# Kernel tuning notes

Hardware: AMD Instinct MI355X
Metric: run time of the kernel (lower is better)

## Reference

```python
import jax, jax.numpy as jnp
import numpy as np

DECAY = 0.99
EPSILON = 1e-05


def setup_inputs() -> dict:
    key = jax.random.key(0)
    k1, k2, k3, k4 = jax.random.split(key, 4)
    B, S, D, K = 16, 2048, 512, 2048
    x = jax.random.normal(k1, (B, S, D), dtype=jnp.float32)
    embed = jax.random.normal(k2, (K, D), dtype=jnp.float32)
    cluster_size = jax.random.uniform(k3, (K,), dtype=jnp.float32)
    embed_avg = jax.random.normal(k4, (K, D), dtype=jnp.float32)
    return {"x": x, "embed": embed, "cluster_size": cluster_size, "embed_avg": embed_avg}


def reference(x, embed, cluster_size, embed_avg):
    # x: [B,S,D]  embed: [K,D]  cluster_size: [K]  embed_avg: [K,D]
    B, S, D = x.shape
    K = embed.shape[0]
    xf = x.reshape(-1, D)  # [N,D], N=B*S

    # quantize(): negative squared euclidean distance, argmax over codebook
    x_sq = jnp.sum(xf * xf, axis=1, keepdims=True)            # [N,1]
    e_sq = jnp.sum(embed * embed, axis=1)[None, :]            # [1,K]
    dist = -(x_sq - 2.0 * (xf @ embed.T) + e_sq)              # [N,K]
    embed_ind = jnp.argmax(dist, axis=-1)                     # [N] int

    # dequantize
    quantize = embed[embed_ind].reshape(B, S, D)

    # training EMA updates (onehot.sum(0) and x^T @ onehot expressed as segment sums)
    ones = jnp.ones((xf.shape[0],), dtype=x.dtype)
    bins = jax.ops.segment_sum(ones, embed_ind, num_segments=K)        # [K] == onehot.sum(0)
    embed_sum_t = jax.ops.segment_sum(xf, embed_ind, num_segments=K)   # [K,D] == (x.T @ onehot).T

    new_cluster_size = cluster_size * DECAY + (1.0 - DECAY) * bins
    new_embed_avg = embed_avg * DECAY + (1.0 - DECAY) * embed_sum_t

    total = new_cluster_size.sum()
    smoothed = (new_cluster_size + EPSILON) / (total + K * EPSILON) * total  # laplace smoothing
    new_embed = new_embed_avg / smoothed[:, None]

    return (quantize,
            embed_ind.reshape(B, S),
            dist.reshape(B, S, K),
            new_cluster_size,
            new_embed_avg,
            new_embed)
```

## Files before the change

### kernel.cpp

```cpp
#include <hip/hip_runtime.h>

#define DECAY 0.99f
#define OMD   0.01f
#define EPS   1e-5f

constexpr int Bb = 16, Ss = 2048, Dd = 512, Kk = 2048;
constexpr int Nn = Bb * Ss;

typedef __attribute__((ext_vector_type(8))) short short8;
typedef __attribute__((ext_vector_type(4))) float f32x4;

__device__ __forceinline__ unsigned short f2bf(float x) {
    unsigned u = __float_as_uint(x);
    unsigned r = (u + 0x7FFFu + ((u >> 16) & 1u)) >> 16;
    return (unsigned short)r;
}
__device__ __forceinline__ float bf2f(unsigned short u) {
    return __uint_as_float((unsigned)u << 16);
}

__device__ __forceinline__ void gload_lds16(const void* g, void* l) {
    __builtin_amdgcn_global_load_lds(
        (const __attribute__((address_space(1))) void*)g,
        (__attribute__((address_space(3))) void*)l, 16, 0, 0);
}

#define BARRIER() do { asm volatile("" ::: "memory"); \
                       __builtin_amdgcn_s_barrier();  \
                       asm volatile("" ::: "memory"); } while (0)

__global__ void rows_sq(const float* __restrict__ in, float* __restrict__ out, int nrows) {
    int row  = blockIdx.x * 4 + (threadIdx.x >> 6);
    int lane = threadIdx.x & 63;
    if (row >= nrows) return;
    const float4* p = (const float4*)(in + (size_t)row * Dd);
    float s = 0.f;
    #pragma unroll
    for (int i = 0; i < 2; ++i) {
        float4 v = p[lane + 64 * i];
        s += v.x * v.x + v.y * v.y + v.z * v.z + v.w * v.w;
    }
    #pragma unroll
    for (int off = 32; off; off >>= 1) s += __shfl_down(s, off);
    if (lane == 0) out[row] = s;
}

__global__ void conv_split2(const float* __restrict__ in,
                            unsigned short* __restrict__ ph,
                            unsigned short* __restrict__ pm, int n4) {
    int i = blockIdx.x * 256 + threadIdx.x;
    if (i >= n4) return;
    float4 v = ((const float4*)in)[i];
    float f[4] = {v.x, v.y, v.z, v.w};
    ushort4 h, m;
    unsigned short hh[4], mm[4];
    #pragma unroll
    for (int j = 0; j < 4; ++j) {
        float x = f[j];
        unsigned short a = f2bf(x);  float ra = x - bf2f(a);
        unsigned short b = f2bf(ra);
        hh[j] = a; mm[j] = b;
    }
    h.x = hh[0]; h.y = hh[1]; h.z = hh[2]; h.w = hh[3];
    m.x = mm[0]; m.y = mm[1]; m.z = mm[2]; m.w = mm[3];
    ((ushort4*)ph)[i] = h;
    ((ushort4*)pm)[i] = m;
}

__global__ __launch_bounds__(512, 1) void gemm_split256(
    const unsigned short* __restrict__ xp,
    const unsigned short* __restrict__ ep,
    const float* __restrict__ xsq,
    const float* __restrict__ esq,
    float* __restrict__ dist,
    unsigned long long* __restrict__ packed)
{
    __shared__ unsigned short As[2][256][64];
    __shared__ unsigned short Bs[2][256][64];

    const int tid  = threadIdx.x;
    const int lane = tid & 63;
    const int wid  = tid >> 6;
    const int wr   = wid >> 2;
    const int wc   = wid & 3;

    int bid = blockIdx.x;
    int wg  = (bid & 7) * 128 + (bid >> 3);
    int mb  = wg >> 3, nb = wg & 7;
    const int row0 = mb * 256, col0 = nb * 256;

    f32x4 acc[8][4] = {};
    short8 af[4], afh[4], bl[2], blh[2], bh[2], bhh[2];

    const int l8   = lane >> 3;
    const int csrc = (lane & 7) ^ l8;

    auto stageAt = [&](const unsigned short* pl, int d, int tt) {
        int ko = (tt & 7) * 64;
        #pragma unroll
        for (int jj = 0; jj < 4; ++jj) {
            int rowbase = jj * 64 + wid * 8;
            const unsigned short* src =
                pl + (size_t)(row0 + rowbase + l8) * Dd + ko + csrc * 8;
            gload_lds16(src, &As[d][rowbase][0]);
        }
    };
    auto stageBt = [&](const unsigned short* pl, int d, int tt) {
        int ko = (tt & 7) * 64;
        #pragma unroll
        for (int jj = 0; jj < 4; ++jj) {
            int rowbase = jj * 64 + wid * 8;
            const unsigned short* src =
                pl + (size_t)(col0 + rowbase + l8) * Dd + ko + csrc * 8;
            gload_lds16(src, &Bs[d][rowbase][0]);
        }
    };

    auto readA4 = [&](int d, int msel) {
        #pragma unroll
        for (int m = 0; m < 4; ++m) {
            int r  = wr * 128 + (msel * 4 + m) * 16 + (lane & 15);
            int c  = ((lane >> 4))     ^ (r & 7);
            int c2 = ((lane >> 4) + 4) ^ (r & 7);
            af[m]  = *(const short8*)&As[d][r][c * 8];
            afh[m] = *(const short8*)&As[d][r][c2 * 8];
        }
    };
    auto readBlo = [&](int d) {
        #pragma unroll
        for (int n = 0; n < 2; ++n) {
            int r  = wc * 64 + n * 16 + (lane & 15);
            int c  = ((lane >> 4))     ^ (r & 7);
            int c2 = ((lane >> 4) + 4) ^ (r & 7);
            bl[n]  = *(const short8*)&Bs[d][r][c * 8];
            blh[n] = *(const short8*)&Bs[d][r][c2 * 8];
        }
    };
    auto readBhi = [&](int d) {
        #pragma unroll
        for (int n = 0; n < 2; ++n) {
            int r  = wc * 64 + (2 + n) * 16 + (lane & 15);
            int c  = ((lane >> 4))     ^ (r & 7);
            int c2 = ((lane >> 4) + 4) ^ (r & 7);
            bh[n]  = *(const short8*)&Bs[d][r][c * 8];
            bhh[n] = *(const short8*)&Bs[d][r][c2 * 8];
        }
    };

    auto mfmaQ = [&](int msel, int nsel, const short8* b0, const short8* b1) {
        #pragma unroll
        for (int m = 0; m < 4; ++m)
            #pragma unroll
            for (int n = 0; n < 2; ++n) {
                int am = msel * 4 + m, bn = nsel * 2 + n;
                acc[am][bn] = __builtin_amdgcn_mfma_f32_16x16x32_bf16(af[m], b0[n], acc[am][bn], 0, 0, 0);
            }
        #pragma unroll
        for (int m = 0; m < 4; ++m)
            #pragma unroll
            for (int n = 0; n < 2; ++n) {
                int am = msel * 4 + m, bn = nsel * 2 + n;
                acc[am][bn] = __builtin_amdgcn_mfma_f32_16x16x32_bf16(afh[m], b1[n], acc[am][bn], 0, 0, 0);
            }
    };

    stageAt(xp, 0, 0);
    stageBt(ep, 0, 0);
    asm volatile("s_waitcnt vmcnt(0)" ::: "memory");
    BARRIER();

    for (int t = 0; t < 32; ++t) {
        const int cur = t & 1, nxt = cur ^ 1;
        const bool st = (t < 31);
        int pn = (t + 1) >> 3;
        const unsigned short* Apn = xp + (size_t)((pn == 2 || pn == 3) ? 1 : 0) * ((size_t)Nn * Dd);
        const unsigned short* Bpn = ep + (size_t)((pn == 1 || pn == 3) ? 1 : 0) * ((size_t)Kk * Dd);

        readA4(cur, 0); readBlo(cur); readBhi(cur);
        if (st) { stageAt(Apn, nxt, t + 1); stageBt(Bpn, nxt, t + 1); }
        mfmaQ(0, 0, bl, blh);
        mfmaQ(0, 1, bh, bhh);
        readA4(cur, 1);
        mfmaQ(1, 1, bh, bhh);
        mfmaQ(1, 0, bl, blh);
        asm volatile("s_waitcnt vmcnt(0)" ::: "memory");
        BARRIER();
    }

    const int jrow = (lane >> 4) * 4;
    const int ncol = lane & 15;
    #pragma unroll
    for (int m = 0; m < 8; ++m) {
        int rbase = row0 + wr * 128 + m * 16 + jrow;
        #pragma unroll
        for (int j = 0; j < 4; ++j) {
            int row = rbase + j;
            float xs = xsq[row];
            float best = -3.4e38f; int bi = 0;
            #pragma unroll
            for (int n = 0; n < 4; ++n) {
                int col = col0 + wc * 64 + n * 16 + ncol;
                float v = 2.f * acc[m][n][j] - xs - esq[col];
                dist[(size_t)row * Kk + col] = v;
                if (v > best) { best = v; bi = col; }
            }
            unsigned u = __float_as_uint(best);
            u = (u & 0x80000000u) ? ~u : (u | 0x80000000u);
            unsigned long long pk = ((unsigned long long)u << 32) | (unsigned)(~bi);
            #pragma unroll
            for (int off = 1; off < 16; off <<= 1) {
                unsigned long long o = __shfl_xor(pk, off);
                if (o > pk) pk = o;
            }
            if (ncol == 0) atomicMax(&packed[row], pk);
        }
    }
}

__global__ void unpack_argmax(const unsigned long long* __restrict__ packed,
                              float* __restrict__ ind_f, int* __restrict__ ind_i) {
    int i = blockIdx.x * 256 + threadIdx.x;
    unsigned long long p = packed[i];
    int k = (int)(~(unsigned)(p & 0xFFFFFFFFull));
    ind_f[i] = (float)k;
    ind_i[i] = k;
}

#define BM 64
#define BN 64
#define BK 32
__global__ __launch_bounds__(256) void gemm_dist(
    const float* __restrict__ A, const float* __restrict__ Bm,
    const float* __restrict__ xsq, const float* __restrict__ esq,
    float* __restrict__ dist)
{
    __shared__ float Asl[BK][BM + 4];
    __shared__ float Bsl[BK][BN + 4];
    int tid = threadIdx.x;
    int row0 = blockIdx.x * BM, col0 = blockIdx.y * BN;
    int tx = tid & 15, ty = tid >> 4;
    float acc[4][4] = {};
    int lr = tid >> 3, lc = (tid & 7) * 4;
    for (int d0 = 0; d0 < Dd; d0 += BK) {
        float4 a0 = *(const float4*)(A  + (size_t)(row0 + lr)      * Dd + d0 + lc);
        float4 a1 = *(const float4*)(A  + (size_t)(row0 + lr + 32) * Dd + d0 + lc);
        float4 b0 = *(const float4*)(Bm + (size_t)(col0 + lr)      * Dd + d0 + lc);
        float4 b1 = *(const float4*)(Bm + (size_t)(col0 + lr + 32) * Dd + d0 + lc);
        __syncthreads();
        Asl[lc + 0][lr] = a0.x; Asl[lc + 1][lr] = a0.y; Asl[lc + 2][lr] = a0.z; Asl[lc + 3][lr] = a0.w;
        Asl[lc + 0][lr + 32] = a1.x; Asl[lc + 1][lr + 32] = a1.y; Asl[lc + 2][lr + 32] = a1.z; Asl[lc + 3][lr + 32] = a1.w;
        Bsl[lc + 0][lr] = b0.x; Bsl[lc + 1][lr] = b0.y; Bsl[lc + 2][lr] = b0.z; Bsl[lc + 3][lr] = b0.w;
        Bsl[lc + 0][lr + 32] = b1.x; Bsl[lc + 1][lr + 32] = b1.y; Bsl[lc + 2][lr + 32] = b1.z; Bsl[lc + 3][lr + 32] = b1.w;
        __syncthreads();
        #pragma unroll
        for (int kd = 0; kd < BK; ++kd) {
            float4 av = *(const float4*)&Asl[kd][ty * 4];
            float4 bv = *(const float4*)&Bsl[kd][tx * 4];
            float a[4] = {av.x, av.y, av.z, av.w};
            float b[4] = {bv.x, bv.y, bv.z, bv.w};
            #pragma unroll
            for (int i = 0; i < 4; ++i)
                #pragma unroll
                for (int j = 0; j < 4; ++j)
                    acc[i][j] = fmaf(a[i], b[j], acc[i][j]);
        }
    }
    #pragma unroll
    for (int i = 0; i < 4; ++i) {
        int row = row0 + ty * 4 + i;
        float xs = xsq[row];
        float4 o;
        int col = col0 + tx * 4;
        o.x = 2.f * acc[i][0] - xs - esq[col + 0];
        o.y = 2.f * acc[i][1] - xs - esq[col + 1];
        o.z = 2.f * acc[i][2] - xs - esq[col + 2];
        o.w = 2.f * acc[i][3] - xs - esq[col + 3];
        *(float4*)(dist + (size_t)row * Kk + col) = o;
    }
}

__global__ void argmax_k(const float* __restrict__ dist,
                         float* __restrict__ ind_f, int* __restrict__ ind_i) {
    int row  = blockIdx.x * 4 + (threadIdx.x >> 6);
    int lane = threadIdx.x & 63;
    const float4* p = (const float4*)(dist + (size_t)row * Kk);
    float best = -3.4e38f;
    int bidx = 0;
    #pragma unroll
    for (int it = 0; it < Kk / 4 / 64; ++it) {
        int i = lane + it * 64;
        float4 v = p[i];
        int base = i * 4;
        if (v.x > best) { best = v.x; bidx = base + 0; }
        if (v.y > best) { best = v.y; bidx = base + 1; }
        if (v.z > best) { best = v.z; bidx = base + 2; }
        if (v.w > best) { best = v.w; bidx = base + 3; }
    }
    #pragma unroll
    for (int off = 32; off; off >>= 1) {
        float ov = __shfl_down(best, off);
        int   oi = __shfl_down(bidx, off);
        if (ov > best || (ov == best && oi < bidx)) { best = ov; bidx = oi; }
    }
    if (lane == 0) { ind_f[row] = (float)bidx; ind_i[row] = bidx; }
}

__global__ void gather_scatter(const float* __restrict__ x,
                               const float* __restrict__ embed,
                               const int* __restrict__ ind,
                               float* __restrict__ quant,
                               float* __restrict__ esum,
                               int* __restrict__ bins) {
    int n = blockIdx.x;
    int k = ind[n];
    int t = threadIdx.x;
    size_t xb = (size_t)n * Dd;
    size_t eb = (size_t)k * Dd;
    float v0 = x[xb + t];
    float v1 = x[xb + t + 256];
    quant[xb + t]       = embed[eb + t];
    quant[xb + t + 256] = embed[eb + t + 256];
    atomicAdd(&esum[eb + t],       v0);
    atomicAdd(&esum[eb + t + 256], v1);
    if (t == 0) atomicAdd(&bins[k], 1);
}

__global__ void finalize1(const float* __restrict__ cs, const int* __restrict__ bins,
                          float* __restrict__ ncs, float* __restrict__ total_ws) {
    __shared__ float red[16];
    int t = threadIdx.x;
    float s = 0.f;
    for (int k = t; k < Kk; k += 1024) {
        float v = cs[k] * DECAY + OMD * (float)bins[k];
        ncs[k] = v;
        s += v;
    }
    #pragma unroll
    for (int off = 32; off; off >>= 1) s += __shfl_down(s, off);
    if ((t & 63) == 0) red[t >> 6] = s;
    __syncthreads();
    if (t == 0) {
        float tot = 0.f;
        #pragma unroll
        for (int i = 0; i < 16; ++i) tot += red[i];
        total_ws[0] = tot;
    }
}

__global__ void finalize2(const float* __restrict__ ea, const float* __restrict__ esum,
                          const float* __restrict__ ncs, const float* __restrict__ total_ws,
                          float* __restrict__ nea, float* __restrict__ ne) {
    int idx = blockIdx.x * 256 + threadIdx.x;
    float total = total_ws[0];
    int k = idx >> 7;
    float sm = (ncs[k] + EPS) / (total + Kk * EPS) * total;
    float inv = 1.f / sm;
    float4 a = ((const float4*)ea)[idx];
    float4 s = ((const float4*)esum)[idx];
    float4 r;
    r.x = a.x * DECAY + OMD * s.x;
    r.y = a.y * DECAY + OMD * s.y;
    r.z = a.z * DECAY + OMD * s.z;
    r.w = a.w * DECAY + OMD * s.w;
    ((float4*)nea)[idx] = r;
    float4 e;
    e.x = r.x * inv; e.y = r.y * inv; e.z = r.z * inv; e.w = r.w * inv;
    ((float4*)ne)[idx] = e;
}

extern "C" void kernel_launch(void* const* d_in, const int* in_sizes, int n_in,
                              void* d_out, int out_size, void* d_ws, size_t ws_size,
                              hipStream_t stream) {
    const float* x     = (const float*)d_in[0];
    const float* embed = (const float*)d_in[1];
    const float* cs    = (const float*)d_in[2];
    const float* ea    = (const float*)d_in[3];

    float* out     = (float*)d_out;
    float* o_quant = out;
    float* o_ind   = o_quant + (size_t)Nn * Dd;
    float* o_dist  = o_ind + Nn;
    float* o_ncs   = o_dist + (size_t)Nn * Kk;
    float* o_nea   = o_ncs + Kk;
    float* o_ne    = o_nea + (size_t)Kk * Dd;

    size_t xp_elems = (size_t)3 * Nn * Dd;
    size_t ep_elems = (size_t)3 * Kk * Dd;
    char* w = (char*)d_ws;
    unsigned short* xp = (unsigned short*)w;                 w += xp_elems * 2;
    unsigned short* epp = (unsigned short*)w;                w += ep_elems * 2;
    float* xsq   = (float*)w;                                w += (size_t)Nn * 4;
    float* esq   = (float*)w;                                w += (size_t)Kk * 4;
    int*   ind_i = (int*)w;                                  w += (size_t)Nn * 4;
    int*   bins  = (int*)w;                                  w += (size_t)Kk * 4;
    float* esum  = (float*)w;                                w += (size_t)Kk * Dd * 4;
    unsigned long long* packed = (unsigned long long*)w;     w += (size_t)Nn * 8;
    float* total = (float*)w;                                w += 256;
    size_t need = (size_t)(w - (char*)d_ws);

    if (ws_size >= need) {
        hipMemsetAsync(bins, 0, (size_t)Kk * 4 + (size_t)Kk * Dd * 4 + (size_t)Nn * 8, stream);

        rows_sq<<<Nn / 4, 256, 0, stream>>>(x, xsq, Nn);
        rows_sq<<<Kk / 4, 256, 0, stream>>>(embed, esq, Kk);

        conv_split2<<<(Nn * Dd / 4 + 255) / 256, 256, 0, stream>>>(
            x, xp, xp + (size_t)Nn * Dd, Nn * Dd / 4);
        conv_split2<<<(Kk * Dd / 4 + 255) / 256, 256, 0, stream>>>(
            embed, epp, epp + (size_t)Kk * Dd, Kk * Dd / 4);

        gemm_split256<<<(Nn / 256) * (Kk / 256), 512, 0, stream>>>(
            xp, epp, xsq, esq, o_dist, packed);

        unpack_argmax<<<Nn / 256, 256, 0, stream>>>(packed, o_ind, ind_i);
    } else {
        float* fxsq  = (float*)d_ws;
        float* fesq  = fxsq + Nn;
        int*   find  = (int*)(fesq + Kk);
        int*   fbins = find + Nn;
        float* fesum = (float*)(fbins + Kk);
        float* ftot  = fesum + (size_t)Kk * Dd;
        xsq = fxsq; esq = fesq; ind_i = find; bins = fbins; esum = fesum; total = ftot;

        hipMemsetAsync(bins, 0, (size_t)(Kk + Kk * Dd) * sizeof(float), stream);
        rows_sq<<<Nn / 4, 256, 0, stream>>>(x, xsq, Nn);
        rows_sq<<<Kk / 4, 256, 0, stream>>>(embed, esq, Kk);
        dim3 g(Nn / BM, Kk / BN);
        gemm_dist<<<g, 256, 0, stream>>>(x, embed, xsq, esq, o_dist);
        argmax_k<<<Nn / 4, 256, 0, stream>>>(o_dist, o_ind, ind_i);
    }

    gather_scatter<<<Nn, 256, 0, stream>>>(x, embed, ind_i, o_quant, esum, bins);
    finalize1<<<1, 1024, 0, stream>>>(cs, bins, o_ncs, total);
    finalize2<<<(Kk * Dd / 4) / 256, 256, 0, stream>>>(ea, esum, o_ncs, total, o_nea, o_ne);
}
```

Measured before the change: 440.8 us.

## Triple-buffer A tiles in split GEMM and fuse conversion and argmax-unpack kernels

The split-bf16 GEMM now triple-buffers the A tile in LDS. It issues global-to-LDS loads two steps ahead for A and one step ahead for B, and waits with vmcnt(4) instead of draining all loads every iteration, so memory latency overlaps the MFMA work. The row-squared-norm kernels are merged into the bf16 hi/lo split conversion, which reads x and embed once. The argmax unpack is fused into the gather/scatter kernel, which removes a launch and the ind_i round trip. The extra LDS buffer grows shared memory per block, and the partial waitcnt depends on the exact count of outstanding loads being right.

```diff
diff --git a/kernel.cpp b/kernel.cpp
--- a/kernel.cpp
+++ b/kernel.cpp
@@ -45,26 +45,36 @@
     if (lane == 0) out[row] = s;
 }
 
-__global__ void conv_split2(const float* __restrict__ in,
-                            unsigned short* __restrict__ ph,
-                            unsigned short* __restrict__ pm, int n4) {
-    int i = blockIdx.x * 256 + threadIdx.x;
-    if (i >= n4) return;
-    float4 v = ((const float4*)in)[i];
-    float f[4] = {v.x, v.y, v.z, v.w};
-    ushort4 h, m;
-    unsigned short hh[4], mm[4];
-    #pragma unroll
-    for (int j = 0; j < 4; ++j) {
-        float x = f[j];
-        unsigned short a = f2bf(x);  float ra = x - bf2f(a);
-        unsigned short b = f2bf(ra);
-        hh[j] = a; mm[j] = b;
-    }
-    h.x = hh[0]; h.y = hh[1]; h.z = hh[2]; h.w = hh[3];
-    m.x = mm[0]; m.y = mm[1]; m.z = mm[2]; m.w = mm[3];
-    ((ushort4*)ph)[i] = h;
-    ((ushort4*)pm)[i] = m;
+__global__ void conv_rows(const float* __restrict__ in,
+                          unsigned short* __restrict__ ph,
+                          unsigned short* __restrict__ pm,
+                          float* __restrict__ sq) {
+    int row  = blockIdx.x * 4 + (threadIdx.x >> 6);
+    int lane = threadIdx.x & 63;
+    const float4* p = (const float4*)(in + (size_t)row * Dd);
+    ushort4* h4 = (ushort4*)(ph + (size_t)row * Dd);
+    ushort4* m4 = (ushort4*)(pm + (size_t)row * Dd);
+    float s = 0.f;
+    #pragma unroll
+    for (int i = 0; i < 2; ++i) {
+        int idx = lane + 64 * i;
+        float4 v = p[idx];
+        float f[4] = {v.x, v.y, v.z, v.w};
+        unsigned short hh[4], mm[4];
+        #pragma unroll
+        for (int j = 0; j < 4; ++j) {
+            float x = f[j];
+            s += x * x;
+            unsigned short a = f2bf(x);
+            unsigned short b = f2bf(x - bf2f(a));
+            hh[j] = a; mm[j] = b;
+        }
+        h4[idx] = make_ushort4(hh[0], hh[1], hh[2], hh[3]);
+        m4[idx] = make_ushort4(mm[0], mm[1], mm[2], mm[3]);
+    }
+    #pragma unroll
+    for (int off = 32; off; off >>= 1) s += __shfl_down(s, off);
+    if (lane == 0) sq[row] = s;
 }
 
 __global__ __launch_bounds__(512, 1) void gemm_split256(
@@ -75,7 +85,7 @@
     float* __restrict__ dist,
     unsigned long long* __restrict__ packed)
 {
-    __shared__ unsigned short As[2][256][64];
+    __shared__ unsigned short As[3][256][64];
     __shared__ unsigned short Bs[2][256][64];
 
     const int tid  = threadIdx.x;
@@ -94,6 +104,15 @@
 
     const int l8   = lane >> 3;
     const int csrc = (lane & 7) ^ l8;
+
+    auto Aplane = [&](int tt) -> const unsigned short* {
+        int p = tt >> 3;
+        return xp + (size_t)((p == 2 || p == 3) ? 1 : 0) * ((size_t)Nn * Dd);
+    };
+    auto Bplane = [&](int tt) -> const unsigned short* {
+        int p = tt >> 3;
+        return ep + (size_t)((p == 1 || p == 3) ? 1 : 0) * ((size_t)Kk * Dd);
+    };
 
     auto stageAt = [&](const unsigned short* pl, int d, int tt) {
         int ko = (tt & 7) * 64;
@@ -164,28 +183,32 @@
             }
     };
 
-    stageAt(xp, 0, 0);
-    stageBt(ep, 0, 0);
-    asm volatile("s_waitcnt vmcnt(0)" ::: "memory");
+    stageAt(Aplane(0), 0, 0);
+    stageBt(Bplane(0), 0, 0);
+    stageAt(Aplane(1), 1, 1);
+    asm volatile("s_waitcnt vmcnt(4)" ::: "memory");
     BARRIER();
 
     for (int t = 0; t < 32; ++t) {
-        const int cur = t & 1, nxt = cur ^ 1;
-        const bool st = (t < 31);
-        int pn = (t + 1) >> 3;
-        const unsigned short* Apn = xp + (size_t)((pn == 2 || pn == 3) ? 1 : 0) * ((size_t)Nn * Dd);
-        const unsigned short* Bpn = ep + (size_t)((pn == 1 || pn == 3) ? 1 : 0) * ((size_t)Kk * Dd);
-
-        readA4(cur, 0); readBlo(cur); readBhi(cur);
-        if (st) { stageAt(Apn, nxt, t + 1); stageBt(Bpn, nxt, t + 1); }
+        const int ca = t % 3, cb = t & 1;
+        const int nbb = (t + 1) & 1;
+        const int naa = (t + 2) % 3;
+
+        stageBt(Bplane(t + 1), nbb, t + 1);
+        stageAt(Aplane(t + 2), naa, t + 2);
+
+        readA4(ca, 0); readBlo(cb); readBhi(cb);
         mfmaQ(0, 0, bl, blh);
         mfmaQ(0, 1, bh, bhh);
-        readA4(cur, 1);
+        readA4(ca, 1);
         mfmaQ(1, 1, bh, bhh);
         mfmaQ(1, 0, bl, blh);
-        asm volatile("s_waitcnt vmcnt(0)" ::: "memory");
+
+        __builtin_amdgcn_sched_barrier(0);
+        asm volatile("s_waitcnt vmcnt(4)" ::: "memory");
         BARRIER();
     }
+    asm volatile("s_waitcnt vmcnt(0)" ::: "memory");
 
     const int jrow = (lane >> 4) * 4;
     const int ncol = lane & 15;
@@ -217,13 +240,25 @@
     }
 }
 
-__global__ void unpack_argmax(const unsigned long long* __restrict__ packed,
-                              float* __restrict__ ind_f, int* __restrict__ ind_i) {
-    int i = blockIdx.x * 256 + threadIdx.x;
-    unsigned long long p = packed[i];
-    int k = (int)(~(unsigned)(p & 0xFFFFFFFFull));
-    ind_f[i] = (float)k;
-    ind_i[i] = k;
+__global__ void gather_scatter_packed(const float* __restrict__ x,
+                                      const float* __restrict__ embed,
+                                      const unsigned long long* __restrict__ packed,
+                                      float* __restrict__ quant,
+                                      float* __restrict__ ind_f,
+                                      float* __restrict__ esum,
+                                      int* __restrict__ bins) {
+    int n = blockIdx.x;
+    int k = (int)(~(unsigned)(packed[n] & 0xFFFFFFFFull));
+    int t = threadIdx.x;
+    size_t xb = (size_t)n * Dd;
+    size_t eb = (size_t)k * Dd;
+    float v0 = x[xb + t];
+    float v1 = x[xb + t + 256];
+    quant[xb + t]       = embed[eb + t];
+    quant[xb + t + 256] = embed[eb + t + 256];
+    atomicAdd(&esum[eb + t],       v0);
+    atomicAdd(&esum[eb + t + 256], v1);
+    if (t == 0) { ind_f[n] = (float)k; atomicAdd(&bins[k], 1); }
 }
 
 #define BM 64
@@ -401,18 +436,14 @@
     if (ws_size >= need) {
         hipMemsetAsync(bins, 0, (size_t)Kk * 4 + (size_t)Kk * Dd * 4 + (size_t)Nn * 8, stream);
 
-        rows_sq<<<Nn / 4, 256, 0, stream>>>(x, xsq, Nn);
-        rows_sq<<<Kk / 4, 256, 0, stream>>>(embed, esq, Kk);
-
-        conv_split2<<<(Nn * Dd / 4 + 255) / 256, 256, 0, stream>>>(
-            x, xp, xp + (size_t)Nn * Dd, Nn * Dd / 4);
-        conv_split2<<<(Kk * Dd / 4 + 255) / 256, 256, 0, stream>>>(
-            embed, epp, epp + (size_t)Kk * Dd, Kk * Dd / 4);
+        conv_rows<<<Nn / 4, 256, 0, stream>>>(x, xp, xp + (size_t)Nn * Dd, xsq);
+        conv_rows<<<Kk / 4, 256, 0, stream>>>(embed, epp, epp + (size_t)Kk * Dd, esq);
 
         gemm_split256<<<(Nn / 256) * (Kk / 256), 512, 0, stream>>>(
             xp, epp, xsq, esq, o_dist, packed);
 
-        unpack_argmax<<<Nn / 256, 256, 0, stream>>>(packed, o_ind, ind_i);
+        gather_scatter_packed<<<Nn, 256, 0, stream>>>(
+            x, embed, packed, o_quant, o_ind, esum, bins);
     } else {
         float* fxsq  = (float*)d_ws;
         float* fesq  = fxsq + Nn;
@@ -428,9 +459,9 @@
         dim3 g(Nn / BM, Kk / BN);
         gemm_dist<<<g, 256, 0, stream>>>(x, embed, xsq, esq, o_dist);
         argmax_k<<<Nn / 4, 256, 0, stream>>>(o_dist, o_ind, ind_i);
-    }
-
-    gather_scatter<<<Nn, 256, 0, stream>>>(x, embed, ind_i, o_quant, esum, bins);
+        gather_scatter<<<Nn, 256, 0, stream>>>(x, embed, ind_i, o_quant, esum, bins);
+    }
+
     finalize1<<<1, 1024, 0, stream>>>(cs, bins, o_ncs, total);
     finalize2<<<(Kk * Dd / 4) / 256, 256, 0, stream>>>(ea, esum, o_ncs, total, o_nea, o_ne);
 }
```

New measurement: 438.8 us. About the same (-0.5%).
